# Kernel tuning notes

Hardware: AMD Instinct MI355X
Metric: run time of the kernel (lower is better)

## Reference

```python
import math
import jax, jax.numpy as jnp
import numpy as np

HEADS = 8


def setup_inputs() -> dict:
    key = jax.random.key(0)
    ks = jax.random.split(key, 8)
    B, L, S, C = 2, 1024, 2048, 1280
    CORR = 256  # native seg_corr resolution; nearest-upsampled x4 to (1024, 1024)
    sc = 0.02
    return {
        "hidden_states": jax.random.normal(ks[0], (B, L, C), jnp.float32),
        "encoder_hidden_states": jax.random.normal(ks[1], (B, S, C), jnp.float32),
        "seg_corr": jax.random.randint(ks[2], (B, CORR, CORR), 0, 2, jnp.int32),
        "Wq": jax.random.normal(ks[3], (C, C), jnp.float32) * sc,
        "Wk": jax.random.normal(ks[4], (C, C), jnp.float32) * sc,
        "Wv": jax.random.normal(ks[5], (C, C), jnp.float32) * sc,
        "Wo": jax.random.normal(ks[6], (C, C), jnp.float32) * sc,
        "bo": jnp.zeros((C,), jnp.float32),
    }


def reference(hidden_states, encoder_hidden_states, seg_corr, Wq, Wk, Wv, Wo, bo):
    B, L, C = hidden_states.shape
    S = encoder_hidden_states.shape[1]
    H = HEADS
    d = C // H

    # projections -> [B, H, L, d] / [B, H, S, d]
    q = (hidden_states @ Wq).reshape(B, L, H, d).transpose(0, 2, 1, 3)
    k = (encoder_hidden_states @ Wk).reshape(B, S, H, d).transpose(0, 2, 1, 3)
    v = (encoder_hidden_states @ Wv).reshape(B, S, H, d).transpose(0, 2, 1, 3)

    scale = 1.0 / math.sqrt(d)
    scores = jnp.einsum("bhld,bhsd->bhls", q, k) * scale  # [B, H, L, S]

    half = S // 2  # S == 2L in the match-attention branch
    # nearest-neighbor upsample of seg_corr to (L, half) == integer repeat
    rL = L // seg_corr.shape[1]
    rS = half // seg_corr.shape[2]
    corr = jnp.repeat(jnp.repeat(seg_corr, rL, axis=1), rS, axis=2)[:, None]  # [B,1,L,half]

    # hard correlation mask on the second half of keys (reference-image tokens)
    masked = jnp.where(corr == 1, scores[..., half:], jnp.float32(-jnp.inf))
    scores = jnp.concatenate([scores[..., :half], masked], axis=-1)

    attn_weight = jax.nn.softmax(scores, axis=-1)  # dropout_p = 0.0
    out = jnp.einsum("bhls,bhsd->bhld", attn_weight, v)
    out = out.transpose(0, 2, 1, 3).reshape(B, L, C)

    out = out @ Wo + bo            # to_out[0]; to_out[1] dropout is identity at p=0
    out = out + hidden_states      # residual connection; rescale_output_factor = 1
    return out
```

## Files before the change

kernel.cpp:

```cpp
#include <hip/hip_runtime.h>

typedef unsigned short u16;
typedef unsigned int   u32;
typedef unsigned char  u8;

using bf16x8 = __attribute__((ext_vector_type(8))) __bf16;
using f32x4  = __attribute__((ext_vector_type(4))) float;

__device__ __forceinline__ u16 f2bf(float f) {
    u32 u = __float_as_uint(f);
    return (u16)((u + 0x7FFFu + ((u >> 16) & 1u)) >> 16);
}

#define MFMA(a, b, c) __builtin_amdgcn_mfma_f32_16x16x32_bf16((a), (b), (c), 0, 0, 0)
#define EXP2(x) __builtin_amdgcn_exp2f(x)

__device__ __forceinline__ void gll16(const u16* g, u16* l) {
    __builtin_amdgcn_global_load_lds(
        (const __attribute__((address_space(1))) void*)g,
        (__attribute__((address_space(3))) void*)l, 16, 0, 0);
}

__global__ __launch_bounds__(256) void wtrans_kernel(
    const float* __restrict__ W0, const float* __restrict__ W1,
    const float* __restrict__ W2, const float* __restrict__ W3,
    u16* __restrict__ T0, u16* __restrict__ T1,
    u16* __restrict__ T2, u16* __restrict__ T3) {
    const int N = 1280;
    const int z = blockIdx.z;
    const float* W = (z == 0) ? W0 : (z == 1) ? W1 : (z == 2) ? W2 : W3;
    u16* T = (z == 0) ? T0 : (z == 1) ? T1 : (z == 2) ? T2 : T3;
    __shared__ float t[32][33];
    const int bx = blockIdx.x * 32, by = blockIdx.y * 32;
    const int x = threadIdx.x, ty = threadIdx.y;
#pragma unroll
    for (int j = 0; j < 4; j++) {
        const int y = ty + j * 8;
        t[y][x] = W[(size_t)(by + y) * N + (bx + x)];
    }
    __syncthreads();
#pragma unroll
    for (int j = 0; j < 4; j++) {
        const int y = ty + j * 8;
        T[(size_t)(bx + y) * N + (by + x)] = f2bf(t[x][y]);
    }
}

__global__ __launch_bounds__(256) void conv2_kernel(const float* __restrict__ in0,
                                                    u16* __restrict__ out0,
                                                    const float* __restrict__ in1,
                                                    u16* __restrict__ out1) {
    const int bid = blockIdx.x;
    const float* in = (bid < 1280) ? in0 : in1;
    u16* out = (bid < 1280) ? out0 : out1;
    const int i = ((bid < 1280) ? bid : bid - 1280) * 256 + threadIdx.x;
    const float4 a = ((const float4*)in)[i * 2];
    const float4 b = ((const float4*)in)[i * 2 + 1];
    union { uint4 u; u16 s[8]; } cv;
    cv.s[0] = f2bf(a.x); cv.s[1] = f2bf(a.y); cv.s[2] = f2bf(a.z); cv.s[3] = f2bf(a.w);
    cv.s[4] = f2bf(b.x); cv.s[5] = f2bf(b.y); cv.s[6] = f2bf(b.z); cv.s[7] = f2bf(b.w);
    ((uint4*)out)[i] = cv.u;
}

template <int MI, bool TRANSC, bool EPI>
__global__ __launch_bounds__(256) void gemm2_kernel(
    const u16* __restrict__ A, const u16* __restrict__ Bt, void* __restrict__ Cp,
    const float* __restrict__ bias, const float* __restrict__ resid,
    const int M, const int N, const int K) {
    __shared__ __align__(16) u16 Al[2][MI * 32 * 64];
    __shared__ __align__(16) u16 Bl[2][128 * 64];
    const int tid = threadIdx.x;
    const int lane = tid & 63, w = tid >> 6;
    const int wr = w >> 1, wc = w & 1;
    const int lr = lane & 15, lq = lane >> 4;
    const int m0 = blockIdx.y * (MI * 32), n0 = blockIdx.x * 128;

    const int f_r = tid >> 3;
    const int srcch = (tid & 7) ^ ((tid >> 3) & 7);
    const int ldst = (tid & 192) * 8;

    const f32x4 fzero = {0.f, 0.f, 0.f, 0.f};
    f32x4 acc[MI][4];
#pragma unroll
    for (int i = 0; i < MI; i++)
#pragma unroll
        for (int j = 0; j < 4; j++) acc[i][j] = fzero;

    const int nkt = K >> 6;

#define STAGE(buf, kt)                                                          \
    {                                                                           \
        const int k0s = (kt) << 6;                                              \
        _Pragma("unroll")                                                       \
        for (int i = 0; i < MI; i++) {                                          \
            const int r = i * 32 + f_r;                                         \
            gll16(&A[(size_t)(m0 + r) * K + k0s + srcch * 8],                   \
                  &Al[buf][i * 2048 + ldst]);                                   \
        }                                                                       \
        _Pragma("unroll")                                                       \
        for (int i = 0; i < 4; i++) {                                           \
            const int r = i * 32 + f_r;                                         \
            gll16(&Bt[(size_t)(n0 + r) * K + k0s + srcch * 8],                  \
                  &Bl[buf][i * 2048 + ldst]);                                   \
        }                                                                       \
    }

    STAGE(0, 0);
    asm volatile("s_waitcnt vmcnt(0)" ::: "memory");
    __syncthreads();
    int cur = 0;
    for (int kt = 0; kt < nkt; kt++) {
        if (kt + 1 < nkt) STAGE(cur ^ 1, kt + 1);
#pragma unroll
        for (int ks = 0; ks < 2; ks++) {
            bf16x8 af[MI], bfv[4];
#pragma unroll
            for (int mi = 0; mi < MI; mi++) {
                const int rowA = wr * (MI * 16) + mi * 16 + lr;
                af[mi] = *(const bf16x8*)&Al[cur][rowA * 64 +
                                                  (((ks * 4 + lq) ^ (rowA & 7)) << 3)];
            }
#pragma unroll
            for (int ni = 0; ni < 4; ni++) {
                const int rowB = wc * 64 + ni * 16 + lr;
                bfv[ni] = *(const bf16x8*)&Bl[cur][rowB * 64 +
                                                   (((ks * 4 + lq) ^ (rowB & 7)) << 3)];
            }
#pragma unroll
            for (int mi = 0; mi < MI; mi++)
#pragma unroll
                for (int ni = 0; ni < 4; ni++)
                    acc[mi][ni] = MFMA(af[mi], bfv[ni], acc[mi][ni]);
        }
        asm volatile("s_waitcnt vmcnt(0)" ::: "memory");
        __syncthreads();
        cur ^= 1;
    }
#undef STAGE

#pragma unroll
    for (int mi = 0; mi < MI; mi++)
#pragma unroll
        for (int ni = 0; ni < 4; ni++)
#pragma unroll
            for (int j = 0; j < 4; j++) {
                const int row = m0 + wr * (MI * 16) + mi * 16 + lq * 4 + j;
                const int col = n0 + wc * 64 + ni * 16 + lr;
                const float v = acc[mi][ni][j];
                if (EPI) {
                    ((float*)Cp)[(size_t)row * N + col] =
                        v + bias[col] + resid[(size_t)row * N + col];
                } else if (TRANSC) {
                    ((u16*)Cp)[((size_t)(col >> 11) * 1280 + row) * 2048 +
                               (col & 2047)] = f2bf(v);
                } else {
                    ((u16*)Cp)[(size_t)row * N + col] = f2bf(v);
                }
            }
}

__global__ __launch_bounds__(256) void attn_kernel(
    const u16* __restrict__ qb, const u16* __restrict__ kb,
    const u16* __restrict__ vtb, const int* __restrict__ seg,
    u16* __restrict__ ao) {
    __shared__ __align__(16) u16 arena[27136];
    const int VT = 5376;
    const int PT = 23552;
    const int SG = 26112;
    u8* segl8 = (u8*)&arena[SG];

    const int tid = threadIdx.x;
    const int lane = tid & 63, w = tid >> 6;
    const int qg = w >> 1, kc = w & 1;
    const int lr = lane & 15, lq = lane >> 4;
    const int id = blockIdx.x;
    const int h = id & 7, bz = (id >> 3) & 1, qt = id >> 4;

#pragma unroll
    for (int i = 0; i < 2; i++) {
        const int4 v =
            *(const int4*)&seg[(size_t)(bz * 256 + qt * 8) * 256 + tid * 8 + i * 4];
        segl8[tid * 8 + i * 4 + 0] = (u8)v.x;
        segl8[tid * 8 + i * 4 + 1] = (u8)v.y;
        segl8[tid * 8 + i * 4 + 2] = (u8)v.z;
        segl8[tid * 8 + i * 4 + 3] = (u8)v.w;
    }

    bf16x8 qf[5];
    {
        const size_t qrow =
            (size_t)(bz * 1024 + qt * 32 + qg * 16 + lr) * 1280 + h * 160;
#pragma unroll
        for (int ks = 0; ks < 5; ks++)
            qf[ks] = *(const bf16x8*)&qb[qrow + ks * 32 + lq * 8];
    }

    const int nk0 = tid, nk1 = tid + 256;
    const int nv0 = tid, nv1 = tid + 256;
    const bool exK = (tid < 128);
    const int ne = exK ? (512 + tid) : (384 + tid);
    const int gok0 = (nk0 / 20) * 1280 + (nk0 % 20) * 8;
    const int lok0 = (nk0 / 20) * 168 + (nk0 % 20) * 8;
    const int gok1 = (nk1 / 20) * 1280 + (nk1 % 20) * 8;
    const int lok1 = (nk1 / 20) * 168 + (nk1 % 20) * 8;
    const int gov0 = (nv0 >> 2) * 2048 + (nv0 & 3) * 8;
    const int lov0 = VT + (nv0 >> 2) * 40 + (nv0 & 3) * 8;
    const int gov1 = (nv1 >> 2) * 2048 + (nv1 & 3) * 8;
    const int lov1 = VT + (nv1 >> 2) * 40 + (nv1 & 3) * 8;
    const int goe = exK ? ((ne / 20) * 1280 + (ne % 20) * 8)
                        : ((ne >> 2) * 2048 + (ne & 3) * 8);
    const int loe = exK ? ((ne / 20) * 168 + (ne % 20) * 8)
                        : (VT + (ne >> 2) * 40 + (ne & 3) * 8);

    const u16* kP = kb + (size_t)(bz * 2048) * 1280 + h * 160;
    const u16* vP = vtb + (size_t)(bz * 1280 + h * 160) * 2048;

    const f32x4 fzero = {0.f, 0.f, 0.f, 0.f};
    f32x4 oacc[5];
#pragma unroll
    for (int d = 0; d < 5; d++) oacc[d] = fzero;
    f32x4 oaccL = fzero;
    const float sc2 = 0.11405508f;
    bf16x8 ones8;
#pragma unroll
    for (int e = 0; e < 8; e++) {
        const u16 one = 0x3F80;
        ones8[e] = *(const __bf16*)&one;
    }
    u16* ptw = &arena[PT + w * 640];

    uint4 rk0 = *(const uint4*)&kP[gok0];
    uint4 rk1 = *(const uint4*)&kP[gok1];
    uint4 rv0 = *(const uint4*)&vP[gov0];
    uint4 rv1 = *(const uint4*)&vP[gov1];
    uint4 re  = exK ? *(const uint4*)&kP[goe] : *(const uint4*)&vP[goe];
    *(uint4*)&arena[lok0] = rk0;
    *(uint4*)&arena[lok1] = rk1;
    *(uint4*)&arena[lov0] = rv0;
    *(uint4*)&arena[lov1] = rv1;
    if (exK) *(uint4*)&arena[loe] = re;
    else     *(uint4*)&arena[loe] = re;
    kP += 40960;
    vP += 32;
    __syncthreads();

    int cb = 0;
    for (int kt = 0; kt < 64; kt++) {
        if (kt + 1 < 64) {
            rk0 = *(const uint4*)&kP[gok0];
            rk1 = *(const uint4*)&kP[gok1];
            rv0 = *(const uint4*)&vP[gov0];
            rv1 = *(const uint4*)&vP[gov1];
            re  = exK ? *(const uint4*)&kP[goe] : *(const uint4*)&vP[goe];
            kP += 40960;
            vP += 32;
        }

        const u16* kbase = &arena[cb + lr * 168 + lq * 8];
        f32x4 s0 = fzero, s1 = fzero;
#pragma unroll
        for (int ks = 0; ks < 5; ks++) {
            s0 = MFMA(qf[ks], *(const bf16x8*)&kbase[ks * 32], s0);
            s1 = MFMA(qf[ks], *(const bf16x8*)&kbase[16 * 168 + ks * 32], s1);
        }

        float msk0 = 0.f, msk1 = 0.f;
        if (kt >= 32) {
            const int sgb = (kt - 32) * 8 + (lr >> 2);
            const int qrow4 = (qg * 4 + lq) * 256;
            msk0 = segl8[qrow4 + sgb] ? 0.f : -1e30f;
            msk1 = segl8[qrow4 + sgb + 4] ? 0.f : -1e30f;
        }
#pragma unroll
        for (int j = 0; j < 4; j++) {
            const float p0 = EXP2(fmaf(s0[j], sc2, msk0));
            const float p1 = EXP2(fmaf(s1[j], sc2, msk1));
            *(__bf16*)&ptw[(lq * 4 + j) * 40 + lr] = (__bf16)p0;
            *(__bf16*)&ptw[(lq * 4 + j) * 40 + 16 + lr] = (__bf16)p1;
        }

        const bf16x8 pa = *(const bf16x8*)&ptw[lr * 40 + lq * 8];
        oaccL = MFMA(pa, ones8, oaccL);
#pragma unroll
        for (int nt2 = 0; nt2 < 5; nt2++) {
            const bf16x8 bv = *(const bf16x8*)
                &arena[cb + VT + (kc * 80 + nt2 * 16 + lr) * 40 + lq * 8];
            oacc[nt2] = MFMA(pa, bv, oacc[nt2]);
        }

        if (kt + 1 < 64) {
            const int nb = cb ^ 11776;
            *(uint4*)&arena[nb + lok0] = rk0;
            *(uint4*)&arena[nb + lok1] = rk1;
            *(uint4*)&arena[nb + lov0] = rv0;
            *(uint4*)&arena[nb + lov1] = rv1;
            *(uint4*)&arena[nb + loe] = re;
        }
        __syncthreads();
        cb ^= 11776;
    }

    float inv[4];
#pragma unroll
    for (int j = 0; j < 4; j++) inv[j] = 1.f / oaccL[j];
#pragma unroll
    for (int nt2 = 0; nt2 < 5; nt2++)
#pragma unroll
        for (int j = 0; j < 4; j++) {
            const int row = qt * 32 + qg * 16 + lq * 4 + j;
            const int col = h * 160 + kc * 80 + nt2 * 16 + lr;
            *(__bf16*)&ao[(size_t)(bz * 1024 + row) * 1280 + col] =
                (__bf16)(oacc[nt2][j] * inv[j]);
        }
}

extern "C" void kernel_launch(void* const* d_in, const int* in_sizes, int n_in,
                              void* d_out, int out_size, void* d_ws, size_t ws_size,
                              hipStream_t stream) {
    const float* hs  = (const float*)d_in[0];
    const float* ehs = (const float*)d_in[1];
    const int*   seg = (const int*)d_in[2];
    const float* Wq  = (const float*)d_in[3];
    const float* Wk  = (const float*)d_in[4];
    const float* Wv  = (const float*)d_in[5];
    const float* Wo  = (const float*)d_in[6];
    const float* bo  = (const float*)d_in[7];
    float* out = (float*)d_out;

    u16* base  = (u16*)d_ws;
    u16* WoT   = base;
    u16* qbuf  = WoT + 1638400;
    u16* kbuf  = qbuf + 2621440;
    u16* vtbuf = kbuf + 5242880;
    u16* hbuf  = vtbuf + 5242880;
    u16* ebuf  = hbuf + 2621440;
    u16* WqT   = ebuf + 5242880;
    u16* WkT   = WqT + 1638400;
    u16* WvT   = WkT + 1638400;
    u16* aobuf = hbuf;

    dim3 tb(32, 8), tg(40, 40, 4);
    wtrans_kernel<<<tg, tb, 0, stream>>>(Wq, Wk, Wv, Wo, WqT, WkT, WvT, WoT);
    conv2_kernel<<<3840, 256, 0, stream>>>(hs, hbuf, ehs, ebuf);

    gemm2_kernel<1, false, false><<<dim3(10, 64), 256, 0, stream>>>(
        hbuf, WqT, qbuf, nullptr, nullptr, 2048, 1280, 1280);
    gemm2_kernel<2, false, false><<<dim3(10, 64), 256, 0, stream>>>(
        ebuf, WkT, kbuf, nullptr, nullptr, 4096, 1280, 1280);
    gemm2_kernel<2, true, false><<<dim3(32, 20), 256, 0, stream>>>(
        WvT, ebuf, vtbuf, nullptr, nullptr, 1280, 4096, 1280);

    attn_kernel<<<512, 256, 0, stream>>>(qbuf, kbuf, vtbuf, seg, aobuf);

    gemm2_kernel<1, false, true><<<dim3(10, 64), 256, 0, stream>>>(
        aobuf, WoT, out, bo, hs, 2048, 1280, 1280);
}
```

Measured before the change: 169.7 us.

## Split QK^T score computation between paired waves sharing a P tile

Each pair of waves with the same query group now computes only half of the 32-key score tile (16 keys each) instead of both redundantly computing all 32. The exponentiated probabilities are written into a shared per-query-group LDS tile, and an extra block barrier lets both waves read the full P tile for the PV MFMAs. This halves the QK MFMA and exp work per wave and shrinks LDS use. The cost is a second __syncthreads per iteration, and the score accumulation is split into two independent chains that are summed.

Result: faster. 160.9 us (-5.2%).

```diff
diff --git a/kernel.cpp b/kernel.cpp
--- a/kernel.cpp
+++ b/kernel.cpp
@@ -163,10 +163,10 @@
     const u16* __restrict__ qb, const u16* __restrict__ kb,
     const u16* __restrict__ vtb, const int* __restrict__ seg,
     u16* __restrict__ ao) {
-    __shared__ __align__(16) u16 arena[27136];
+    __shared__ __align__(16) u16 arena[25856];
     const int VT = 5376;
     const int PT = 23552;
-    const int SG = 26112;
+    const int SG = 24832;
     u8* segl8 = (u8*)&arena[SG];
 
     const int tid = threadIdx.x;
@@ -227,7 +227,7 @@
         const u16 one = 0x3F80;
         ones8[e] = *(const __bf16*)&one;
     }
-    u16* ptw = &arena[PT + w * 640];
+    u16* ptq = &arena[PT + qg * 640];
 
     uint4 rk0 = *(const uint4*)&kP[gok0];
     uint4 rk1 = *(const uint4*)&kP[gok1];
@@ -238,8 +238,7 @@
     *(uint4*)&arena[lok1] = rk1;
     *(uint4*)&arena[lov0] = rv0;
     *(uint4*)&arena[lov1] = rv1;
-    if (exK) *(uint4*)&arena[loe] = re;
-    else     *(uint4*)&arena[loe] = re;
+    *(uint4*)&arena[loe] = re;
     kP += 40960;
     vP += 32;
     __syncthreads();
@@ -256,30 +255,27 @@
             vP += 32;
         }
 
-        const u16* kbase = &arena[cb + lr * 168 + lq * 8];
-        f32x4 s0 = fzero, s1 = fzero;
-#pragma unroll
-        for (int ks = 0; ks < 5; ks++) {
-            s0 = MFMA(qf[ks], *(const bf16x8*)&kbase[ks * 32], s0);
-            s1 = MFMA(qf[ks], *(const bf16x8*)&kbase[16 * 168 + ks * 32], s1);
-        }
-
-        float msk0 = 0.f, msk1 = 0.f;
+        const u16* kbase = &arena[cb + (kc * 16 + lr) * 168 + lq * 8];
+        f32x4 sA = fzero, sB = fzero;
+        sA = MFMA(qf[0], *(const bf16x8*)&kbase[0],   sA);
+        sB = MFMA(qf[1], *(const bf16x8*)&kbase[32],  sB);
+        sA = MFMA(qf[2], *(const bf16x8*)&kbase[64],  sA);
+        sB = MFMA(qf[3], *(const bf16x8*)&kbase[96],  sB);
+        sA = MFMA(qf[4], *(const bf16x8*)&kbase[128], sA);
+
+        float msk = 0.f;
         if (kt >= 32) {
-            const int sgb = (kt - 32) * 8 + (lr >> 2);
-            const int qrow4 = (qg * 4 + lq) * 256;
-            msk0 = segl8[qrow4 + sgb] ? 0.f : -1e30f;
-            msk1 = segl8[qrow4 + sgb + 4] ? 0.f : -1e30f;
+            const int sg = (kt - 32) * 8 + kc * 4 + (lr >> 2);
+            msk = segl8[(qg * 4 + lq) * 256 + sg] ? 0.f : -1e30f;
         }
 #pragma unroll
         for (int j = 0; j < 4; j++) {
-            const float p0 = EXP2(fmaf(s0[j], sc2, msk0));
-            const float p1 = EXP2(fmaf(s1[j], sc2, msk1));
-            *(__bf16*)&ptw[(lq * 4 + j) * 40 + lr] = (__bf16)p0;
-            *(__bf16*)&ptw[(lq * 4 + j) * 40 + 16 + lr] = (__bf16)p1;
-        }
-
-        const bf16x8 pa = *(const bf16x8*)&ptw[lr * 40 + lq * 8];
+            const float e = EXP2(fmaf(sA[j] + sB[j], sc2, msk));
+            *(__bf16*)&ptq[(lq * 4 + j) * 40 + kc * 16 + lr] = (__bf16)e;
+        }
+        __syncthreads();
+
+        const bf16x8 pa = *(const bf16x8*)&ptq[lr * 40 + lq * 8];
         oaccL = MFMA(pa, ones8, oaccL);
 #pragma unroll
         for (int nt2 = 0; nt2 < 5; nt2++) {
```
